# Optimization experiments

Measured on AMD Instinct MI355X. Metric: run time of the kernel, lower is better.

Reference implementation:

```python
import jax, jax.numpy as jnp
import numpy as np

BIG = 1000000.0


def setup_inputs() -> dict:
    key = jax.random.key(0)
    k1, k2 = jax.random.split(key)
    embeddings = jax.random.normal(k1, (8192, 128), dtype=jnp.float32)
    labels = jax.random.randint(k2, (8192,), 0, 512, dtype=jnp.int64)
    return {"embeddings": embeddings, "labels": labels, "margin": jnp.float32(0.5)}


def _pairwise_euclidean(x):
    # [N, N] Euclidean distance matrix, numerically safe sqrt (zero diag)
    sq = jnp.sum(x * x, axis=1)
    d2 = sq[:, None] + sq[None, :] - 2.0 * (x @ x.T)
    d2 = jnp.maximum(d2, 0.0)
    nz = d2 > 0.0
    return jnp.where(nz, jnp.sqrt(jnp.where(nz, d2, 1.0)), 0.0)


def reference(embeddings, labels, margin):
    n = embeddings.shape[0]
    dist = _pairwise_euclidean(embeddings)                      # [N, N]
    same = (labels[:, None] == labels[None, :]).astype(dist.dtype)
    mask_pos = same - jnp.eye(n, dtype=dist.dtype)              # positives, excl. self
    mask_neg = 1.0 - same                                       # different label
    pos_dist = jnp.max(dist * mask_pos, axis=1)                 # hardest positive
    neg_dist = jnp.min(dist + (1.0 - mask_neg) * BIG, axis=1)   # hardest negative
    loss = jax.nn.relu(pos_dist - neg_dist + margin)
    return jnp.mean(loss)
```

## Files before the change

### kernel.cpp

```cpp
#include <hip/hip_runtime.h>

#define NROW 8192
#define DIM  128
#define NSEG 16
#define BIGF 1e30f

typedef __attribute__((ext_vector_type(8))) short bf16x8;
typedef __attribute__((ext_vector_type(4))) float f32x4;


__device__ __forceinline__ unsigned short f2bf(float f) {
    unsigned u = __float_as_uint(f);
    unsigned r = (u + 0x7fffu + ((u >> 16) & 1u)) >> 16;
    return (unsigned short)r;
}

__device__ __forceinline__ void gload_lds16(const void* g, void* l) {
    __builtin_amdgcn_global_load_lds(
        (const __attribute__((address_space(1))) void*)g,
        (__attribute__((address_space(3))) void*)l, 16, 0, 0);
}

__global__ __launch_bounds__(256) void prep_kernel(const float* __restrict__ x,
                                                   unsigned short* __restrict__ xb2,
                                                   float* __restrict__ sq,
                                                   float* __restrict__ out) {
    int gtid = blockIdx.x * 256 + threadIdx.x;
    if (gtid == 0) out[0] = 0.0f;
    int row  = gtid >> 6;
    int lane = threadIdx.x & 63;
    const float* xr = x + (size_t)row * DIM;
    float a = xr[lane];
    float b = xr[lane + 64];
    size_t d0 = (size_t)(row >> 4) * 2048 + (size_t)(lane >> 3) * 128
              + (size_t)(row & 15) * 8 + (lane & 7);
    xb2[d0]            = f2bf(a);
    xb2[d0 + 8 * 128]  = f2bf(b);
    float s = a * a + b * b;
    #pragma unroll
    for (int o = 32; o > 0; o >>= 1) s += __shfl_down(s, o);
    if (lane == 0) sq[row] = s;
}

__global__ __launch_bounds__(256, 3) void tile_mfma(const unsigned short* __restrict__ xb2,
                                                    const int* __restrict__ lbl,
                                                    const float* __restrict__ sq,
                                                    float* __restrict__ posS,
                                                    float* __restrict__ negS) {
    __shared__ unsigned short Bs[2][64 * DIM];
    const int bid = blockIdx.x;
    const int rb  = bid >> 4;
    const int jq  = bid & 15;
    const int i0  = rb * 128;
    const int jbase = jq * 512;
    const int t    = threadIdx.x;
    const int lane = t & 63;
    const int w    = t >> 6;
    const int wr0  = i0 + w * 32;
    const int quad = lane >> 4;
    const int l15  = lane & 15;

    const char* xbB = (const char*)xb2;

    bf16x8 af[2][4];
    const int gA = wr0 >> 4;
    #pragma unroll
    for (int ti = 0; ti < 2; ti++)
        #pragma unroll
        for (int ks = 0; ks < 4; ks++)
            af[ti][ks] = *(const bf16x8*)(xb2 + (size_t)(gA + ti) * 2048 + (ks * 4 + quad) * 128 + l15 * 8);

    int lbli[2][4];
    #pragma unroll
    for (int ti = 0; ti < 2; ti++) {
        int4 l4 = *(const int4*)(lbl + wr0 + ti * 16 + quad * 4);
        lbli[ti][0] = l4.x; lbli[ti][1] = l4.y; lbli[ti][2] = l4.z; lbli[ti][3] = l4.w;
    }
    const bool hasDiag = (i0 >= jbase) && (i0 < jbase + 512);

    float posm[2][4], negm[2][4];
    #pragma unroll
    for (int ti = 0; ti < 2; ti++)
        #pragma unroll
        for (int r = 0; r < 4; r++) { posm[ti][r] = -BIGF; negm[ti][r] = BIGF; }

    {
        const char* src = xbB + (size_t)(jbase >> 4) * 4096;
        #pragma unroll
        for (int i = 0; i < 4; i++)
            gload_lds16(src + i * 4096 + t * 16, (char*)&Bs[0][0] + i * 4096 + w * 1024);
    }
    __syncthreads();

    #pragma unroll 1
    for (int jt = 0; jt < 8; jt++) {
        const int cur = jt & 1;
        const int j0  = jbase + jt * 64;

        if (jt < 7) {
            const char* src = xbB + (size_t)((j0 + 64) >> 4) * 4096;
            #pragma unroll
            for (int i = 0; i < 4; i++)
                gload_lds16(src + i * 4096 + t * 16, (char*)&Bs[cur ^ 1][0] + i * 4096 + w * 1024);
        }

        float sqj[4]; int lblj[4];
        #pragma unroll
        for (int tj = 0; tj < 4; tj++) {
            int c = j0 + tj * 16 + l15;
            sqj[tj]  = sq[c];
            lblj[tj] = lbl[c];
        }

        f32x4 acc[2][4];
        #pragma unroll
        for (int ti = 0; ti < 2; ti++)
            #pragma unroll
            for (int tj = 0; tj < 4; tj++) acc[ti][tj] = (f32x4){0.f, 0.f, 0.f, 0.f};

        #pragma unroll
        for (int ks = 0; ks < 4; ks++) {
            bf16x8 bfr[4];
            #pragma unroll
            for (int tj = 0; tj < 4; tj++)
                bfr[tj] = *(const bf16x8*)((const char*)&Bs[cur][0] + tj * 4096 + (ks * 4 + quad) * 256 + l15 * 16);
            #pragma unroll
            for (int ti = 0; ti < 2; ti++)
                #pragma unroll
                for (int tj = 0; tj < 4; tj++)
                    acc[ti][tj] = __builtin_amdgcn_mfma_f32_16x16x32_bf16(af[ti][ks], bfr[tj], acc[ti][tj], 0, 0, 0);
        }

        #pragma unroll
        for (int ti = 0; ti < 2; ti++) {
            const int rowg = wr0 + ti * 16 + quad * 4;
            #pragma unroll
            for (int tj = 0; tj < 4; tj++) {
                const int jc = j0 + tj * 16 + l15;
                #pragma unroll
                for (int r = 0; r < 4; r++) {
                    float sr = fmaf(-2.0f, acc[ti][tj][r], sqj[tj]);
                    bool same = (lbli[ti][r] == lblj[tj]);
                    bool self = hasDiag && (jc == rowg + r);
                    posm[ti][r] = fmaxf(posm[ti][r], (same && !self) ? sr : -BIGF);
                    negm[ti][r] = fminf(negm[ti][r], same ? BIGF : sr);
                }
            }
        }

        __syncthreads();
    }

    #pragma unroll
    for (int ti = 0; ti < 2; ti++)
        #pragma unroll
        for (int r = 0; r < 4; r++) {
            float p = posm[ti][r];
            float n = negm[ti][r];
            #pragma unroll
            for (int m = 8; m >= 1; m >>= 1) {
                p = fmaxf(p, __shfl_xor(p, m));
                n = fminf(n, __shfl_xor(n, m));
            }
            if (l15 == 0) {
                int row = wr0 + ti * 16 + quad * 4 + r;
                float sqi = sq[row];
                posS[jq * NROW + row] = fmaxf(0.0f, sqi + p);
                negS[jq * NROW + row] = fmaxf(0.0f, sqi + n);
            }
        }
}

__global__ __launch_bounds__(256) void tri_final(const float* __restrict__ posS,
                                                 const float* __restrict__ negS,
                                                 const float* __restrict__ margin,
                                                 float* __restrict__ out) {
    int r = blockIdx.x * 256 + threadIdx.x;
    float p = 0.0f, n = BIGF;
    #pragma unroll
    for (int q = 0; q < NSEG; q++) {
        p = fmaxf(p, posS[q * NROW + r]);
        n = fminf(n, negS[q * NROW + r]);
    }
    float m = margin[0];
    float loss = fmaxf(sqrtf(p) - sqrtf(n) + m, 0.0f) * (1.0f / (float)NROW);
    #pragma unroll
    for (int o = 32; o > 0; o >>= 1) loss += __shfl_down(loss, o);
    __shared__ float wsum[4];
    int lane = threadIdx.x & 63, wv = threadIdx.x >> 6;
    if (lane == 0) wsum[wv] = loss;
    __syncthreads();
    if (threadIdx.x == 0) atomicAdd(out, wsum[0] + wsum[1] + wsum[2] + wsum[3]);
}

extern "C" void kernel_launch(void* const* d_in, const int* in_sizes, int n_in,
                              void* d_out, int out_size, void* d_ws, size_t ws_size,
                              hipStream_t stream) {
    const float* x      = (const float*)d_in[0];
    const int*   lbl    = (const int*)d_in[1];
    const float* margin = (const float*)d_in[2];
    float* out = (float*)d_out;

    char* ws = (char*)d_ws;
    unsigned short* xb2 = (unsigned short*)ws;
    float* sq   = (float*)(ws + (2u << 20));
    float* posS = (float*)(ws + (2u << 20) + (64u << 10));
    float* negS = (float*)(ws + (2u << 20) + (576u << 10));

    prep_kernel<<<2048, 256, 0, stream>>>(x, xb2, sq, out);
    tile_mfma<<<64 * NSEG, 256, 0, stream>>>(xb2, lbl, sq, posS, negS);
    tri_final<<<NROW / 256, 256, 0, stream>>>(posS, negS, margin, out);
}
```

Baseline: 90.08 us.

## Sort rows by label so same-label pairs form bands and skip mask logic

```diff
diff --git a/kernel.cpp b/kernel.cpp
--- a/kernel.cpp
+++ b/kernel.cpp
@@ -2,7 +2,9 @@
 
 #define NROW 8192
 #define DIM  128
+#define NLBL 512
 #define NSEG 16
+#define NBLK (64 * NSEG)
 #define BIGF 1e30f
 
 typedef __attribute__((ext_vector_type(8))) short bf16x8;
@@ -21,30 +23,76 @@
         (__attribute__((address_space(3))) void*)l, 16, 0, 0);
 }
 
-__global__ __launch_bounds__(256) void prep_kernel(const float* __restrict__ x,
-                                                   unsigned short* __restrict__ xb2,
-                                                   float* __restrict__ sq,
+__global__ __launch_bounds__(512) void zero_hist(int* __restrict__ hist) {
+    hist[threadIdx.x] = 0;
+}
+
+__global__ __launch_bounds__(256) void hist_kernel(const int* __restrict__ lbl,
+                                                   int* __restrict__ hist) {
+    int i = blockIdx.x * 256 + threadIdx.x;
+    atomicAdd(&hist[lbl[i]], 1);
+}
+
+__global__ __launch_bounds__(512) void scan_kernel(const int* __restrict__ hist,
+                                                   int* __restrict__ binStart,
+                                                   unsigned* __restrict__ cursor,
                                                    float* __restrict__ out) {
-    int gtid = blockIdx.x * 256 + threadIdx.x;
-    if (gtid == 0) out[0] = 0.0f;
-    int row  = gtid >> 6;
-    int lane = threadIdx.x & 63;
-    const float* xr = x + (size_t)row * DIM;
-    float a = xr[lane];
-    float b = xr[lane + 64];
-    size_t d0 = (size_t)(row >> 4) * 2048 + (size_t)(lane >> 3) * 128
-              + (size_t)(row & 15) * 8 + (lane & 7);
-    xb2[d0]            = f2bf(a);
-    xb2[d0 + 8 * 128]  = f2bf(b);
-    float s = a * a + b * b;
-    #pragma unroll
-    for (int o = 32; o > 0; o >>= 1) s += __shfl_down(s, o);
-    if (lane == 0) sq[row] = s;
+    __shared__ int sc[NLBL];
+    const int t = threadIdx.x;
+    int h = hist[t];
+    sc[t] = h;
+    __syncthreads();
+    for (int off = 1; off < NLBL; off <<= 1) {
+        int v = (t >= off) ? sc[t - off] : 0;
+        __syncthreads();
+        sc[t] += v;
+        __syncthreads();
+    }
+    int st = sc[t] - h;
+    binStart[t] = st;
+    cursor[t]   = (unsigned)st;
+    if (t == 0) { binStart[NLBL] = NROW; out[0] = 0.0f; }
+}
+
+__global__ __launch_bounds__(256) void prep_scatter(const float* __restrict__ x,
+                                                    const int* __restrict__ lbl,
+                                                    const int* __restrict__ binStart,
+                                                    unsigned* __restrict__ cursor,
+                                                    unsigned short* __restrict__ xb2,
+                                                    float* __restrict__ sq,
+                                                    unsigned* __restrict__ rowBand,
+                                                    int* __restrict__ lblS) {
+    const int t   = threadIdx.x;
+    const int row = blockIdx.x * 16 + (t >> 4);
+    const int c   = t & 15;
+    const float* xr = x + (size_t)row * DIM + c * 8;
+    float4 f0 = *(const float4*)xr;
+    float4 f1 = *(const float4*)(xr + 4);
+    float s = f0.x*f0.x + f0.y*f0.y + f0.z*f0.z + f0.w*f0.w
+            + f1.x*f1.x + f1.y*f1.y + f1.z*f1.z + f1.w*f1.w;
+    #pragma unroll
+    for (int m = 1; m <= 8; m <<= 1) s += __shfl_xor(s, m);
+    const int l = lbl[row];
+    unsigned p = 0;
+    if (c == 0) p = atomicAdd(&cursor[l], 1u);
+    p = __shfl((int)p, t & 48);
+    unsigned w0 = (unsigned)f2bf(f0.x) | ((unsigned)f2bf(f0.y) << 16);
+    unsigned w1 = (unsigned)f2bf(f0.z) | ((unsigned)f2bf(f0.w) << 16);
+    unsigned w2 = (unsigned)f2bf(f1.x) | ((unsigned)f2bf(f1.y) << 16);
+    unsigned w3 = (unsigned)f2bf(f1.z) | ((unsigned)f2bf(f1.w) << 16);
+    uint4 v = make_uint4(w0, w1, w2, w3);
+    *(uint4*)(xb2 + (size_t)(p >> 4) * 2048 + c * 128 + (p & 15) * 8) = v;
+    if (c == 0) {
+        sq[p]      = s;
+        lblS[p]    = l;
+        rowBand[p] = (unsigned)binStart[l] | ((unsigned)binStart[l + 1] << 16);
+    }
 }
 
 __global__ __launch_bounds__(256, 3) void tile_mfma(const unsigned short* __restrict__ xb2,
-                                                    const int* __restrict__ lbl,
+                                                    const int* __restrict__ lblS,
                                                     const float* __restrict__ sq,
+                                                    const unsigned* __restrict__ rowBand,
                                                     float* __restrict__ posS,
                                                     float* __restrict__ negS) {
     __shared__ unsigned short Bs[2][64 * DIM];
@@ -73,10 +121,25 @@
     int lbli[2][4];
     #pragma unroll
     for (int ti = 0; ti < 2; ti++) {
-        int4 l4 = *(const int4*)(lbl + wr0 + ti * 16 + quad * 4);
+        int4 l4 = *(const int4*)(lblS + wr0 + ti * 16 + quad * 4);
         lbli[ti][0] = l4.x; lbli[ti][1] = l4.y; lbli[ti][2] = l4.z; lbli[ti][3] = l4.w;
     }
-    const bool hasDiag = (i0 >= jbase) && (i0 < jbase + 512);
+    int tiLo[2], tiHi[2];
+    #pragma unroll
+    for (int ti = 0; ti < 2; ti++) {
+        uint4 b4 = *(const uint4*)(rowBand + wr0 + ti * 16 + quad * 4);
+        int lo = (int)(b4.x & 0xffffu), hi = (int)(b4.x >> 16);
+        lo = min(lo, (int)(b4.y & 0xffffu)); hi = max(hi, (int)(b4.y >> 16));
+        lo = min(lo, (int)(b4.z & 0xffffu)); hi = max(hi, (int)(b4.z >> 16));
+        lo = min(lo, (int)(b4.w & 0xffffu)); hi = max(hi, (int)(b4.w >> 16));
+        int v;
+        v = __shfl_xor(lo, 16); lo = min(lo, v);
+        v = __shfl_xor(lo, 32); lo = min(lo, v);
+        v = __shfl_xor(hi, 16); hi = max(hi, v);
+        v = __shfl_xor(hi, 32); hi = max(hi, v);
+        tiLo[ti] = __builtin_amdgcn_readfirstlane(lo);
+        tiHi[ti] = __builtin_amdgcn_readfirstlane(hi);
+    }
 
     float posm[2][4], negm[2][4];
     #pragma unroll
@@ -109,7 +172,7 @@
         for (int tj = 0; tj < 4; tj++) {
             int c = j0 + tj * 16 + l15;
             sqj[tj]  = sq[c];
-            lblj[tj] = lbl[c];
+            lblj[tj] = lblS[c];
         }
 
         f32x4 acc[2][4];
@@ -136,14 +199,23 @@
             const int rowg = wr0 + ti * 16 + quad * 4;
             #pragma unroll
             for (int tj = 0; tj < 4; tj++) {
-                const int jc = j0 + tj * 16 + l15;
-                #pragma unroll
-                for (int r = 0; r < 4; r++) {
-                    float sr = fmaf(-2.0f, acc[ti][tj][r], sqj[tj]);
-                    bool same = (lbli[ti][r] == lblj[tj]);
-                    bool self = hasDiag && (jc == rowg + r);
-                    posm[ti][r] = fmaxf(posm[ti][r], (same && !self) ? sr : -BIGF);
-                    negm[ti][r] = fminf(negm[ti][r], same ? BIGF : sr);
+                const int colLo = j0 + tj * 16;
+                if (colLo + 16 <= tiLo[ti] || colLo >= tiHi[ti]) {
+                    #pragma unroll
+                    for (int r = 0; r < 4; r++) {
+                        float sr = fmaf(-2.0f, acc[ti][tj][r], sqj[tj]);
+                        negm[ti][r] = fminf(negm[ti][r], sr);
+                    }
+                } else {
+                    const int jc = colLo + l15;
+                    #pragma unroll
+                    for (int r = 0; r < 4; r++) {
+                        float sr = fmaf(-2.0f, acc[ti][tj][r], sqj[tj]);
+                        bool same = (lbli[ti][r] == lblj[tj]);
+                        bool self = (jc == rowg + r);
+                        posm[ti][r] = fmaxf(posm[ti][r], (same && !self) ? sr : -BIGF);
+                        negm[ti][r] = fminf(negm[ti][r], same ? BIGF : sr);
+                    }
                 }
             }
         }
@@ -203,11 +275,19 @@
 
     char* ws = (char*)d_ws;
     unsigned short* xb2 = (unsigned short*)ws;
-    float* sq   = (float*)(ws + (2u << 20));
-    float* posS = (float*)(ws + (2u << 20) + (64u << 10));
-    float* negS = (float*)(ws + (2u << 20) + (576u << 10));
-
-    prep_kernel<<<2048, 256, 0, stream>>>(x, xb2, sq, out);
-    tile_mfma<<<64 * NSEG, 256, 0, stream>>>(xb2, lbl, sq, posS, negS);
+    float*    sq       = (float*)(ws + (2u << 20));
+    unsigned* rowBand  = (unsigned*)(ws + (2u << 20) + (32u << 10));
+    int*      lblS     = (int*)(ws + (2u << 20) + (64u << 10));
+    int*      binStart = (int*)(ws + (2u << 20) + (96u << 10));
+    unsigned* cursor   = (unsigned*)(ws + (2u << 20) + (100u << 10));
+    int*      hist     = (int*)(ws + (2u << 20) + (104u << 10));
+    float*    posS     = (float*)(ws + (2u << 20) + (128u << 10));
+    float*    negS     = (float*)(ws + (2u << 20) + (640u << 10));
+
+    zero_hist<<<1, 512, 0, stream>>>(hist);
+    hist_kernel<<<NROW / 256, 256, 0, stream>>>(lbl, hist);
+    scan_kernel<<<1, 512, 0, stream>>>(hist, binStart, cursor, out);
+    prep_scatter<<<NROW / 16, 256, 0, stream>>>(x, lbl, binStart, cursor, xb2, sq, rowBand, lblS);
+    tile_mfma<<<NBLK, 256, 0, stream>>>(xb2, lblS, sq, rowBand, posS, negS);
     tri_final<<<NROW / 256, 256, 0, stream>>>(posS, negS, margin, out);
 }
```

After: 108.4 us. 20.3% more time.
